# Kernel optimization log

Hardware: AMD Instinct MI355X
Metric: run time of the kernel (lower is better)

The kernel has to match this reference:

```python
import jax, jax.numpy as jnp
import numpy as np

EMB = 512
QKV = 512
H = 8      # num_heads
PH = 8     # num_pheads
HD = QKV // H
PHD = QKV // PH


def _make_params(key):
    names = ['Wi', 'Wip', 'Wic', 'Wq', 'Wpq', 'Wk', 'Wpk', 'Wv', 'Wpv', 'Wo', 'Wop']
    ks = jax.random.split(key, len(names))
    p = {}
    for n, k in zip(names, ks):
        din = EMB if n in ('Wi', 'Wip', 'Wic') else QKV
        dout = EMB if n in ('Wo', 'Wop') else QKV
        p[n] = jax.random.normal(k, (din, dout), jnp.float32) * 0.02
        p['b' + n[1:]] = jnp.zeros((dout,), jnp.float32)
    return p


def setup_inputs() -> dict:
    key = jax.random.key(0)
    kq, kp, kc, kw = jax.random.split(key, 4)
    B, S, P = 16, 4096, 64
    inp = {
        'query': jax.random.normal(kq, (B, S, EMB), jnp.float32),
        'pquery': jax.random.normal(kp, (B, P, EMB), jnp.float32),
        'context': jax.random.normal(kc, (B, S, EMB), jnp.float32),
    }
    inp.update(_make_params(kw))
    return inp


def reference(query, pquery, context,
              Wi, bi, Wip, bip, Wic, bic,
              Wq, bq, Wpq, bpq, Wk, bk, Wpk, bpk,
              Wv, bv, Wpv, bpv, Wo, bo, Wop, bop):
    # Dropout layers act as identity (eval mode / deterministic reference).
    B, S, _ = query.shape
    P = pquery.shape[1]

    q_in = query @ Wi + bi        # (B,S,QKV)
    pq_in = pquery @ Wip + bip    # (B,P,QKV)
    c_in = context @ Wic + bic    # (B,S,QKV)

    # --- pack stage: pquery attends over context -> p_context ---
    pq = ((pq_in @ Wpq + bpq) * (PHD ** -0.5)).reshape(B, P, PH, PHD)
    pk = (c_in @ Wpk + bpk).reshape(B, S, PH, PHD)
    pv = (c_in @ Wpv + bpv).reshape(B, S, PH, PHD)
    # dropout before softmax in original; identity here
    pattn = jax.nn.softmax(jnp.einsum('bphd,bshd->bhps', pq, pk), axis=-1)
    pc = jnp.einsum('bhps,bshd->bphd', pattn, pv).reshape(B, P, QKV)

    # --- unpack stage: query attends over p_context ---
    q = ((q_in @ Wq + bq) * (HD ** -0.5)).reshape(B, S, H, HD)
    k = (pc @ Wk + bk).reshape(B, P, H, HD)
    v = (pc @ Wv + bv).reshape(B, P, H, HD)
    aw = jax.nn.softmax(jnp.einsum('bshd,bphd->bhsp', q, k), axis=-1)  # (B,H,S,P)
    attn = jnp.einsum('bhsp,bphd->bshd', aw, v).reshape(B, S, QKV)
    attn = attn @ Wo + bo           # (B,S,EMB)
    pc_out = pc @ Wop + bop         # (B,P,EMB)

    # torch returns attn_weights as (S, B*H, P) when batch_first
    aw_t = jnp.transpose(aw.reshape(B * H, S, P), (1, 0, 2))
    return attn, pc_out, aw_t
```

## Files before the change

### kernel.cpp

```cpp
#include <hip/hip_runtime.h>


typedef __bf16 bf16x8 __attribute__((ext_vector_type(8)));
typedef float f32x4 __attribute__((ext_vector_type(4)));
typedef unsigned short u16x8 __attribute__((ext_vector_type(8)));
typedef unsigned short u16x4 __attribute__((ext_vector_type(4)));

#define MFMA16(a, b, c) __builtin_amdgcn_mfma_f32_16x16x32_bf16((a), (b), (c), 0, 0, 0)

__device__ __forceinline__ unsigned short f2bf_bits(float f) {
  unsigned int u = __float_as_uint(f);
  u += 0x7fffu + ((u >> 16) & 1u);
  return (unsigned short)(u >> 16);
}

__device__ __forceinline__ void gload16(const void* g, void* l) {
  __builtin_amdgcn_global_load_lds(
      (const __attribute__((address_space(1))) void*)g,
      (__attribute__((address_space(3))) void*)l, 16, 0, 0);
}

struct Ptr8 { const float* p[8]; };

__global__ __launch_bounds__(256) void prep_kernel(
    Ptr8 srcs, unsigned short* __restrict__ WT,
    const float* bi, const float* bip, const float* bic,
    const float* Wq, const float* Wpq, const float* Wpk, const float* Wpv,
    const float* bq, const float* bpq, const float* bpk, const float* bpv,
    float* __restrict__ bias_out) {
  const int t = threadIdx.x;
  if (blockIdx.z < 8) {
    const float* __restrict__ W = srcs.p[blockIdx.z];
    unsigned short* __restrict__ O = WT + (size_t)blockIdx.z * 262144;
    __shared__ float tile[32][33];
    const int tr = blockIdx.x * 32, tc = blockIdx.y * 32;
    {
      const int r = t >> 3, c4 = (t & 7) * 4;
      const float4 v = *reinterpret_cast<const float4*>(&W[(size_t)(tr + r) * 512 + tc + c4]);
      tile[r][c4 + 0] = v.x; tile[r][c4 + 1] = v.y; tile[r][c4 + 2] = v.z; tile[r][c4 + 3] = v.w;
    }
    __syncthreads();
    {
      const int n = t >> 3, k4 = (t & 7) * 4;
      u16x4 o;
#pragma unroll
      for (int j = 0; j < 4; j++) o[j] = f2bf_bits(tile[k4 + j][n]);
      *reinterpret_cast<u16x4*>(&O[(size_t)(tc + n) * 512 + tr + k4]) = o;
    }
  } else {
    const int idx = blockIdx.y * 16 + blockIdx.x;
    if (idx >= 8) return;
    const int y = idx >> 1;
    const float* bin  = (y == 0) ? bi : (y == 1) ? bip : bic;
    const float* W    = (y == 0) ? Wq : (y == 1) ? Wpq : (y == 2) ? Wpk : Wpv;
    const float* bout = (y == 0) ? bq : (y == 1) ? bpq : (y == 2) ? bpk : bpv;
    const float scale = (y < 2) ? 0.125f : 1.0f;
    const int n = (idx & 1) * 256 + t;
    float s = 0.f;
    for (int k = 0; k < 512; k++) s += bin[k] * W[(size_t)k * 512 + n];
    bias_out[y * 512 + n] = (s + bout[n]) * scale;
  }
}

__global__ __launch_bounds__(256) void gemm_wcomb(
    const float* __restrict__ Wi, const float* __restrict__ Wip,
    const float* __restrict__ Wic, const unsigned short* __restrict__ WTbase,
    unsigned short* __restrict__ outbase) {
  const int z = blockIdx.z;
  const float* __restrict__ A = (z == 0) ? Wi : (z == 1) ? Wip : Wic;
  const unsigned short* __restrict__ BT = WTbase + (size_t)z * 262144;
  unsigned short* __restrict__ out = outbase + (size_t)z * 262144;
  const float scale = (z < 2) ? 0.125f : 1.0f;

  __shared__ __align__(16) unsigned short As[128 * 72];
  __shared__ __align__(16) unsigned short Bs[128 * 72];
  const int t = threadIdx.x;
  const int w = t >> 6, l = t & 63, li = l & 15, lg = l >> 4;
  const int wm = w >> 1, wn = w & 1;
  const int m0 = blockIdx.x * 128, n0 = blockIdx.y * 128;

  f32x4 acc[4][4] = {};

  for (int kt = 0; kt < 512; kt += 64) {
#pragma unroll
    for (int i = 0; i < 8; i++) {
      const int row = i * 16 + (t >> 4), k = (t & 15) * 4;
      const float4 v = *reinterpret_cast<const float4*>(&A[(size_t)(m0 + row) * 512 + kt + k]);
      u16x4 o;
      o[0] = f2bf_bits(v.x); o[1] = f2bf_bits(v.y);
      o[2] = f2bf_bits(v.z); o[3] = f2bf_bits(v.w);
      *reinterpret_cast<u16x4*>(&As[row * 72 + k]) = o;
    }
#pragma unroll
    for (int i = 0; i < 4; i++) {
      const int row = i * 32 + (t >> 3), k = (t & 7) * 8;
      const u16x8 v = *reinterpret_cast<const u16x8*>(&BT[(size_t)(n0 + row) * 512 + kt + k]);
      *reinterpret_cast<u16x8*>(&Bs[row * 72 + k]) = v;
    }
    __syncthreads();
#pragma unroll
    for (int kk = 0; kk < 2; kk++) {
      bf16x8 a[4], b[4];
#pragma unroll
      for (int mf = 0; mf < 4; mf++)
        a[mf] = *reinterpret_cast<const bf16x8*>(&As[(wm * 64 + mf * 16 + li) * 72 + kk * 32 + lg * 8]);
#pragma unroll
      for (int nf = 0; nf < 4; nf++)
        b[nf] = *reinterpret_cast<const bf16x8*>(&Bs[(wn * 64 + nf * 16 + li) * 72 + kk * 32 + lg * 8]);
#pragma unroll
      for (int mf = 0; mf < 4; mf++)
#pragma unroll
        for (int nf = 0; nf < 4; nf++)
          acc[mf][nf] = MFMA16(a[mf], b[nf], acc[mf][nf]);
    }
    __syncthreads();
  }
  const int lg4 = lg * 4;
#pragma unroll
  for (int nf = 0; nf < 4; nf++) {
    const int col = n0 + wn * 64 + nf * 16 + li;
#pragma unroll
    for (int mf = 0; mf < 4; mf++) {
      const int row = m0 + wm * 64 + mf * 16 + lg4;
#pragma unroll
      for (int r = 0; r < 4; r++)
        out[(size_t)col * 512 + row + r] = f2bf_bits(acc[mf][nf][r] * scale);
    }
  }
}

__global__ __launch_bounds__(256) void gemm_f32lds(
    const float* __restrict__ A, const unsigned short* __restrict__ BT,
    const float* __restrict__ bias0, unsigned short* __restrict__ out0,
    int Ntiles, int ldc) {
  __shared__ __align__(16) float Asf[128 * 64];
  __shared__ __align__(16) unsigned short Bs[128 * 64];
  const int t = threadIdx.x;
  const int w = t >> 6, l = t & 63, li = l & 15, lg = l >> 4;
  const int wm = w >> 1, wn = w & 1;
  const int K = 512;

  const int q8 = gridDim.x >> 3;
  const int wg = (blockIdx.x & 7) * q8 + (blockIdx.x >> 3);
  const int m0 = (wg / Ntiles) * 128, n0 = (wg % Ntiles) * 128;

  f32x4 acc[4][4] = {};

  const int arow = t >> 4, aslot = t & 15;
  const int brow = t >> 3, bslot = t & 7;

  for (int kt = 0; kt < K; kt += 64) {
#pragma unroll
    for (int i = 0; i < 8; i++) {
      const int row = i * 16 + arow;
      const int gs = (aslot ^ (row & 15)) * 4;
      gload16(&A[(size_t)(m0 + row) * K + kt + gs], &Asf[i * 1024 + t * 4]);
    }
#pragma unroll
    for (int i = 0; i < 4; i++) {
      const int row = i * 32 + brow;
      const int gs = (bslot ^ (row & 7)) * 8;
      gload16(&BT[(size_t)(n0 + row) * K + kt + gs], &Bs[(i * 256 + t) * 8]);
    }
    __syncthreads();
#pragma unroll
    for (int kk = 0; kk < 2; kk++) {
      bf16x8 a[4], b[4];
#pragma unroll
      for (int mf = 0; mf < 4; mf++) {
        const int r = wm * 64 + mf * 16 + li;
        const int s0 = kk * 8 + lg * 2;
        const f32x4 lo = *reinterpret_cast<const f32x4*>(&Asf[r * 64 + ((s0 ^ (r & 15)) * 4)]);
        const f32x4 hi = *reinterpret_cast<const f32x4*>(&Asf[r * 64 + (((s0 + 1) ^ (r & 15)) * 4)]);
        bf16x8 v;
#pragma unroll
        for (int j = 0; j < 4; j++) { v[j] = (__bf16)lo[j]; v[j + 4] = (__bf16)hi[j]; }
        a[mf] = v;
      }
#pragma unroll
      for (int nf = 0; nf < 4; nf++) {
        const int r = wn * 64 + nf * 16 + li;
        b[nf] = *reinterpret_cast<const bf16x8*>(&Bs[r * 64 + (((kk * 4 + lg) ^ (r & 7)) * 8)]);
      }
#pragma unroll
      for (int mf = 0; mf < 4; mf++)
#pragma unroll
        for (int nf = 0; nf < 4; nf++)
          acc[mf][nf] = MFMA16(a[mf], b[nf], acc[mf][nf]);
    }
    __syncthreads();
  }

  const int lg4 = lg * 4;
#pragma unroll
  for (int nf = 0; nf < 4; nf++) {
    const int col = n0 + wn * 64 + nf * 16 + li;
    const float bv = bias0[col];
#pragma unroll
    for (int mf = 0; mf < 4; mf++) {
      const int row = m0 + wm * 64 + mf * 16 + lg4;
#pragma unroll
      for (int r = 0; r < 4; r++)
        out0[(size_t)(row + r) * ldc + col] = f2bf_bits(acc[mf][nf][r] + bv);
    }
  }
}

template <int MODE>
__global__ __launch_bounds__(256) void gemm_bf16(
    const unsigned short* __restrict__ A, const unsigned short* __restrict__ BT,
    const float* __restrict__ bias0, const float* __restrict__ bias1,
    const float* __restrict__ bias2, void* out0, void* out1, void* out2,
    int Ntiles, int ldc) {
  __shared__ __align__(16) unsigned short As[128 * 64];
  __shared__ __align__(16) unsigned short Bs[128 * 64];
  const int t = threadIdx.x;
  const int w = t >> 6, l = t & 63, li = l & 15, lg = l >> 4;
  const int wm = w >> 1, wn = w & 1;
  const int K = 512;

  const int q8 = gridDim.x >> 3;
  const int wg = (blockIdx.x & 7) * q8 + (blockIdx.x >> 3);
  const int m0 = (wg / Ntiles) * 128, n0 = (wg % Ntiles) * 128;

  f32x4 acc[4][4] = {};
  const int sr = t >> 3, sslot = t & 7;

  for (int kt = 0; kt < K; kt += 64) {
#pragma unroll
    for (int i = 0; i < 4; i++) {
      const int row = i * 32 + sr;
      const int gs = (sslot ^ (row & 7)) * 8;
      gload16(&A[(size_t)(m0 + row) * K + kt + gs], &As[(i * 256 + t) * 8]);
      gload16(&BT[(size_t)(n0 + row) * K + kt + gs], &Bs[(i * 256 + t) * 8]);
    }
    __syncthreads();
#pragma unroll
    for (int kk = 0; kk < 2; kk++) {
      bf16x8 a[4], b[4];
#pragma unroll
      for (int mf = 0; mf < 4; mf++) {
        const int r = wm * 64 + mf * 16 + li;
        a[mf] = *reinterpret_cast<const bf16x8*>(&As[r * 64 + (((kk * 4 + lg) ^ (r & 7)) * 8)]);
      }
#pragma unroll
      for (int nf = 0; nf < 4; nf++) {
        const int r = wn * 64 + nf * 16 + li;
        b[nf] = *reinterpret_cast<const bf16x8*>(&Bs[r * 64 + (((kk * 4 + lg) ^ (r & 7)) * 8)]);
      }
#pragma unroll
      for (int mf = 0; mf < 4; mf++)
#pragma unroll
        for (int nf = 0; nf < 4; nf++)
          acc[mf][nf] = MFMA16(a[mf], b[nf], acc[mf][nf]);
    }
    __syncthreads();
  }

  const int lg4 = lg * 4;
#pragma unroll
  for (int nf = 0; nf < 4; nf++) {
    const int col = n0 + wn * 64 + nf * 16 + li;
    if constexpr (MODE == 1) {
      float* o = (float*)out0;
      const float bv = bias0[col];
#pragma unroll
      for (int mf = 0; mf < 4; mf++) {
        const int row = m0 + wm * 64 + mf * 16 + lg4;
#pragma unroll
        for (int r = 0; r < 4; r++)
          o[(size_t)(row + r) * ldc + col] = acc[mf][nf][r] + bv;
      }
    } else {
      if (col < 512) {
        unsigned short* o = (unsigned short*)out0;
        const float bv = bias0[col];
#pragma unroll
        for (int mf = 0; mf < 4; mf++) {
          const int row = m0 + wm * 64 + mf * 16 + lg4;
#pragma unroll
          for (int r = 0; r < 4; r++)
            o[(size_t)(row + r) * 512 + col] = f2bf_bits(acc[mf][nf][r] + bv);
        }
      } else if (col < 1024) {
        unsigned short* o = (unsigned short*)out1;
        const float bv = bias1[col - 512];
#pragma unroll
        for (int mf = 0; mf < 4; mf++) {
          const int row = m0 + wm * 64 + mf * 16 + lg4;
#pragma unroll
          for (int r = 0; r < 4; r++)
            o[(size_t)(row + r) * 512 + col - 512] = f2bf_bits(acc[mf][nf][r] + bv);
        }
      } else {
        float* o = (float*)out2;
        const float bv = bias2[col - 1024];
#pragma unroll
        for (int mf = 0; mf < 4; mf++) {
          const int row = m0 + wm * 64 + mf * 16 + lg4;
#pragma unroll
          for (int r = 0; r < 4; r++)
            o[(size_t)(row + r) * 512 + col - 1024] = acc[mf][nf][r] + bv;
        }
      }
    }
  }
}

__global__ __launch_bounds__(256) void gemm_f32a(
    const float* __restrict__ A, const unsigned short* __restrict__ BT,
    const float* __restrict__ bias0, unsigned short* __restrict__ out,
    int K, int ldc) {
  __shared__ __align__(16) unsigned short As[128 * 72];
  __shared__ __align__(16) unsigned short Bs[128 * 72];
  const int t = threadIdx.x;
  const int w = t >> 6, l = t & 63, li = l & 15, lg = l >> 4;
  const int wm = w >> 1, wn = w & 1;
  const int m0 = blockIdx.x * 128, n0 = blockIdx.y * 128;

  f32x4 acc[4][4] = {};

  for (int kt = 0; kt < K; kt += 64) {
#pragma unroll
    for (int i = 0; i < 8; i++) {
      const int row = i * 16 + (t >> 4), k = (t & 15) * 4;
      const float4 v = *reinterpret_cast<const float4*>(&A[(size_t)(m0 + row) * K + kt + k]);
      u16x4 o;
      o[0] = f2bf_bits(v.x); o[1] = f2bf_bits(v.y);
      o[2] = f2bf_bits(v.z); o[3] = f2bf_bits(v.w);
      *reinterpret_cast<u16x4*>(&As[row * 72 + k]) = o;
    }
#pragma unroll
    for (int i = 0; i < 4; i++) {
      const int row = i * 32 + (t >> 3), k = (t & 7) * 8;
      const u16x8 v = *reinterpret_cast<const u16x8*>(&BT[(size_t)(n0 + row) * K + kt + k]);
      *reinterpret_cast<u16x8*>(&Bs[row * 72 + k]) = v;
    }
    __syncthreads();
#pragma unroll
    for (int kk = 0; kk < 2; kk++) {
      bf16x8 a[4], b[4];
#pragma unroll
      for (int mf = 0; mf < 4; mf++)
        a[mf] = *reinterpret_cast<const bf16x8*>(&As[(wm * 64 + mf * 16 + li) * 72 + kk * 32 + lg * 8]);
#pragma unroll
      for (int nf = 0; nf < 4; nf++)
        b[nf] = *reinterpret_cast<const bf16x8*>(&Bs[(wn * 64 + nf * 16 + li) * 72 + kk * 32 + lg * 8]);
#pragma unroll
      for (int mf = 0; mf < 4; mf++)
#pragma unroll
        for (int nf = 0; nf < 4; nf++)
          acc[mf][nf] = MFMA16(a[mf], b[nf], acc[mf][nf]);
    }
    __syncthreads();
  }
  const int lg4 = lg * 4;
#pragma unroll
  for (int nf = 0; nf < 4; nf++) {
    const int col = n0 + wn * 64 + nf * 16 + li;
    const float bv = bias0[col];
#pragma unroll
    for (int mf = 0; mf < 4; mf++) {
      const int row = m0 + wm * 64 + mf * 16 + lg4;
#pragma unroll
      for (int r = 0; r < 4; r++)
        out[(size_t)(row + r) * ldc + col] = f2bf_bits(acc[mf][nf][r] + bv);
    }
  }
}

__global__ __launch_bounds__(256) void pack_attn(
    const unsigned short* __restrict__ pq_buf,
    const unsigned short* __restrict__ pkv_buf, float* __restrict__ partial) {
  __shared__ __align__(16) unsigned short pkL[64 * 72];
  __shared__ __align__(16) unsigned short pvT[64 * 72];
  __shared__ __align__(16) unsigned short prL[4 * 16 * 72];
  const int t = threadIdx.x, w = t >> 6, l = t & 63, li = l & 15, lg = l >> 4;
  const int bh = blockIdx.x, b = bh >> 3, h = bh & 7;
  const int sb = blockIdx.y * 512;

  bf16x8 aq[2];
  {
    const size_t base = ((size_t)(b * 64 + w * 16 + li)) * 512 + h * 64;
    aq[0] = *reinterpret_cast<const bf16x8*>(&pq_buf[base + lg * 8]);
    aq[1] = *reinterpret_cast<const bf16x8*>(&pq_buf[base + 32 + lg * 8]);
  }

  f32x4 acc[4] = {};
  float lsum[4] = {};

  for (int st = 0; st < 8; st++) {
    const int s0 = sb + st * 64;
#pragma unroll
    for (int i = 0; i < 2; i++) {
      const int row = i * 32 + (t >> 3), c = (t & 7) * 8;
      const u16x8 v = *reinterpret_cast<const u16x8*>(
          &pkv_buf[((size_t)(b * 4096 + s0 + row)) * 1024 + h * 64 + c]);
      *reinterpret_cast<u16x8*>(&pkL[row * 72 + c]) = v;
    }
    {
      const int rp = t >> 3, c = (t & 7) * 8;
      const size_t base = ((size_t)(b * 4096 + s0 + 2 * rp)) * 1024 + 512 + h * 64 + c;
      const u16x8 u0 = *reinterpret_cast<const u16x8*>(&pkv_buf[base]);
      const u16x8 u1 = *reinterpret_cast<const u16x8*>(&pkv_buf[base + 1024]);
#pragma unroll
      for (int j = 0; j < 8; j++) {
        const int val = ((int)u0[j] & 0xffff) | ((int)u1[j] << 16);
        *reinterpret_cast<int*>(&pvT[(c + j) * 72 + 2 * rp]) = val;
      }
    }
    __syncthreads();
    f32x4 sc[4] = {};
#pragma unroll
    for (int nf = 0; nf < 4; nf++) {
#pragma unroll
      for (int kk = 0; kk < 2; kk++) {
        const bf16x8 bk = *reinterpret_cast<const bf16x8*>(
            &pkL[(nf * 16 + li) * 72 + kk * 32 + lg * 8]);
        sc[nf] = MFMA16(aq[kk], bk, sc[nf]);
      }
    }
#pragma unroll
    for (int nf = 0; nf < 4; nf++) {
#pragma unroll
      for (int r = 0; r < 4; r++) {
        const float e = __expf(sc[nf][r]);
        lsum[r] += e;
        prL[(w * 16 + lg * 4 + r) * 72 + nf * 16 + li] = f2bf_bits(e);
      }
    }
#pragma unroll
    for (int kk = 0; kk < 2; kk++) {
      const bf16x8 ap = *reinterpret_cast<const bf16x8*>(
          &prL[(w * 16 + li) * 72 + kk * 32 + lg * 8]);
#pragma unroll
      for (int nf = 0; nf < 4; nf++) {
        const bf16x8 bv = *reinterpret_cast<const bf16x8*>(
            &pvT[(nf * 16 + li) * 72 + kk * 32 + lg * 8]);
        acc[nf] = MFMA16(ap, bv, acc[nf]);
      }
    }
    __syncthreads();
  }

#pragma unroll
  for (int m = 1; m < 16; m <<= 1)
#pragma unroll
    for (int r = 0; r < 4; r++) lsum[r] += __shfl_xor(lsum[r], m);

  const size_t pbase = ((size_t)(bh * 8 + blockIdx.y)) * 4160;
#pragma unroll
  for (int nf = 0; nf < 4; nf++)
#pragma unroll
    for (int r = 0; r < 4; r++)
      partial[pbase + (size_t)(w * 16 + lg * 4 + r) * 64 + nf * 16 + li] = acc[nf][r];
  if (li == 0)
#pragma unroll
    for (int r = 0; r < 4; r++) partial[pbase + 4096 + w * 16 + lg * 4 + r] = lsum[r];
}

__global__ __launch_bounds__(256) void pack_combine(const float* __restrict__ partial,
                                                    unsigned short* __restrict__ pc_buf) {
  const int bh = blockIdx.x, b = bh >> 3, h = bh & 7;
  const int t = threadIdx.x;
#pragma unroll
  for (int e = 0; e < 16; e++) {
    const int idx = e * 256 + t;
    const int p = idx >> 6, d = idx & 63;
    float s = 0.f, den = 0.f;
#pragma unroll
    for (int c = 0; c < 8; c++) {
      const float* pb = &partial[((size_t)(bh * 8 + c)) * 4160];
      s += pb[idx];
      den += pb[4096 + p];
    }
    pc_buf[((size_t)(b * 64 + p)) * 512 + h * 64 + d] = f2bf_bits(s / den);
  }
}

__global__ __launch_bounds__(256) void unpack_attn(
    const unsigned short* q_in, const unsigned short* __restrict__ k_buf,
    const unsigned short* __restrict__ v_buf, float* __restrict__ aw_out,
    unsigned short* attnh_out) {
  __shared__ __align__(16) unsigned short kL[64 * 72];
  __shared__ __align__(16) unsigned short vT[64 * 72];
  __shared__ __align__(16) unsigned short prL[4 * 64 * 72];
  const int t = threadIdx.x, w = t >> 6, l = t & 63, li = l & 15, lg = l >> 4;
  const int bh = blockIdx.y, b = bh >> 3, h = bh & 7;
  const int sbase = blockIdx.x * 256 + w * 64;

#pragma unroll
  for (int i = 0; i < 2; i++) {
    const int p = i * 32 + (t >> 3), c = (t & 7) * 8;
    const u16x8 v = *reinterpret_cast<const u16x8*>(
        &k_buf[((size_t)(b * 64 + p)) * 512 + h * 64 + c]);
    *reinterpret_cast<u16x8*>(&kL[p * 72 + c]) = v;
  }
  {
    const int rp = t >> 3, c = (t & 7) * 8;
    const size_t base = ((size_t)(b * 64 + 2 * rp)) * 512 + h * 64 + c;
    const u16x8 u0 = *reinterpret_cast<const u16x8*>(&v_buf[base]);
    const u16x8 u1 = *reinterpret_cast<const u16x8*>(&v_buf[base + 512]);
#pragma unroll
    for (int j = 0; j < 8; j++) {
      const int val = ((int)u0[j] & 0xffff) | ((int)u1[j] << 16);
      *reinterpret_cast<int*>(&vT[(c + j) * 72 + 2 * rp]) = val;
    }
  }
  bf16x8 aq[4][2];
#pragma unroll
  for (int mf = 0; mf < 4; mf++) {
    const size_t base = ((size_t)(b * 4096 + sbase + mf * 16 + li)) * 512 + h * 64;
    aq[mf][0] = *reinterpret_cast<const bf16x8*>(&q_in[base + lg * 8]);
    aq[mf][1] = *reinterpret_cast<const bf16x8*>(&q_in[base + 32 + lg * 8]);
  }
  __syncthreads();

  f32x4 sc[4][4] = {};
#pragma unroll
  for (int kk = 0; kk < 2; kk++)
#pragma unroll
    for (int nf = 0; nf < 4; nf++) {
      const bf16x8 bk = *reinterpret_cast<const bf16x8*>(
          &kL[(nf * 16 + li) * 72 + kk * 32 + lg * 8]);
#pragma unroll
      for (int mf = 0; mf < 4; mf++) sc[mf][nf] = MFMA16(aq[mf][kk], bk, sc[mf][nf]);
    }

#pragma unroll
  for (int mf = 0; mf < 4; mf++) {
#pragma unroll
    for (int r = 0; r < 4; r++) {
      float e[4];
      float rs = 0.f;
#pragma unroll
      for (int nf = 0; nf < 4; nf++) {
        e[nf] = __expf(sc[mf][nf][r]);
        rs += e[nf];
      }
#pragma unroll
      for (int m = 1; m < 16; m <<= 1) rs += __shfl_xor(rs, m);
      const float inv = 1.0f / rs;
      const int srow = sbase + mf * 16 + lg * 4 + r;
#pragma unroll
      for (int nf = 0; nf < 4; nf++) {
        const float pr = e[nf] * inv;
        aw_out[(size_t)srow * 8192 + bh * 64 + nf * 16 + li] = pr;
        prL[(w * 64 + mf * 16 + lg * 4 + r) * 72 + nf * 16 + li] = f2bf_bits(pr);
      }
    }
  }

  f32x4 acc[4][4] = {};
#pragma unroll
  for (int kk = 0; kk < 2; kk++)
#pragma unroll
    for (int mf = 0; mf < 4; mf++) {
      const bf16x8 ap = *reinterpret_cast<const bf16x8*>(
          &prL[(w * 64 + mf * 16 + li) * 72 + kk * 32 + lg * 8]);
#pragma unroll
      for (int nf = 0; nf < 4; nf++) {
        const bf16x8 bv = *reinterpret_cast<const bf16x8*>(
            &vT[(nf * 16 + li) * 72 + kk * 32 + lg * 8]);
        acc[mf][nf] = MFMA16(ap, bv, acc[mf][nf]);
      }
    }
#pragma unroll
  for (int mf = 0; mf < 4; mf++)
#pragma unroll
    for (int nf = 0; nf < 4; nf++)
#pragma unroll
      for (int r = 0; r < 4; r++)
        attnh_out[((size_t)(b * 4096 + sbase + mf * 16 + lg * 4 + r)) * 512 + h * 64 +
                  nf * 16 + li] = f2bf_bits(acc[mf][nf][r]);
}

extern "C" void kernel_launch(void* const* d_in, const int* in_sizes, int n_in,
                              void* d_out, int out_size, void* d_ws, size_t ws_size,
                              hipStream_t stream) {
  (void)in_sizes; (void)n_in; (void)out_size; (void)ws_size;

  const float* query   = (const float*)d_in[0];
  const float* pquery  = (const float*)d_in[1];
  const float* context = (const float*)d_in[2];
  const float* Wi  = (const float*)d_in[3];  const float* bi  = (const float*)d_in[4];
  const float* Wip = (const float*)d_in[5];  const float* bip = (const float*)d_in[6];
  const float* Wic = (const float*)d_in[7];  const float* bic = (const float*)d_in[8];
  const float* Wq  = (const float*)d_in[9];  const float* bq  = (const float*)d_in[10];
  const float* Wpq = (const float*)d_in[11]; const float* bpq = (const float*)d_in[12];
  const float* Wk  = (const float*)d_in[13]; const float* bk  = (const float*)d_in[14];
  const float* Wpk = (const float*)d_in[15]; const float* bpk = (const float*)d_in[16];
  const float* Wv  = (const float*)d_in[17]; const float* bv  = (const float*)d_in[18];
  const float* Wpv = (const float*)d_in[19]; const float* bpv = (const float*)d_in[20];
  const float* Wo  = (const float*)d_in[21]; const float* bo  = (const float*)d_in[22];
  const float* Wop = (const float*)d_in[23]; const float* bop = (const float*)d_in[24];

  char* ws = (char*)d_ws;
  unsigned short* WT     = (unsigned short*)(ws);
  unsigned short* WqeT   = (unsigned short*)(ws + 4u * 1024 * 1024);
  unsigned short* WpqeT  = WqeT + 512 * 512;
  unsigned short* WpkveT = WpqeT + 512 * 512;
  float* bqe   = (float*)(WpkveT + (size_t)1024 * 512);
  float* bpqe  = bqe + 512;
  float* bpkve = bpqe + 512;
  unsigned short* q_buf   = (unsigned short*)(ws + 8u * 1024 * 1024);
  unsigned short* pkv_buf = q_buf + (size_t)65536 * 512;
  unsigned short* pq_buf  = pkv_buf + (size_t)65536 * 1024;
  unsigned short* pc_buf  = pq_buf + (size_t)1024 * 512;
  unsigned short* k_buf   = pc_buf + (size_t)1024 * 512;
  unsigned short* v_buf   = k_buf + (size_t)1024 * 512;
  float* partial = (float*)(v_buf + (size_t)1024 * 512);

  float* out_attn = (float*)d_out;
  float* out_pc   = out_attn + (size_t)16 * 4096 * 512;
  float* out_aw   = out_pc + (size_t)16 * 64 * 512;

  const dim3 blk(256);

  Ptr8 tsrc; tsrc.p[0]=Wq; tsrc.p[1]=Wpq; tsrc.p[2]=Wpk; tsrc.p[3]=Wpv;
  tsrc.p[4]=Wk; tsrc.p[5]=Wv; tsrc.p[6]=Wop; tsrc.p[7]=Wo;
  prep_kernel<<<dim3(16, 16, 9), blk, 0, stream>>>(
      tsrc, WT, bi, bip, bic, Wq, Wpq, Wpk, Wpv, bq, bpq, bpk, bpv, bqe);
  gemm_wcomb<<<dim3(4, 4, 4), blk, 0, stream>>>(Wi, Wip, Wic, WT, WqeT);

  gemm_f32lds<<<dim3(2048), blk, 0, stream>>>(query, WqeT, bqe, q_buf, 4, 512);
  gemm_f32lds<<<dim3(4096), blk, 0, stream>>>(context, WpkveT, bpkve, pkv_buf, 8, 1024);
  gemm_f32a<<<dim3(8, 4), blk, 0, stream>>>(pquery, WpqeT, bpqe, pq_buf, 512, 512);

  pack_attn<<<dim3(128, 8), blk, 0, stream>>>(pq_buf, pkv_buf, partial);
  pack_combine<<<128, blk, 0, stream>>>(partial, pc_buf);

  gemm_bf16<2><<<dim3(96), blk, 0, stream>>>(
      pc_buf, WT + (size_t)4 * 262144, bk, bv, bop, k_buf, v_buf, out_pc, 12, 512);

  unpack_attn<<<dim3(16, 128), blk, 0, stream>>>(q_buf, k_buf, v_buf, out_aw, q_buf);

  gemm_bf16<1><<<dim3(2048), blk, 0, stream>>>(
      q_buf, WT + (size_t)7 * 262144, bo, nullptr, nullptr, out_attn, nullptr, nullptr,
      4, 512);
}
```

Baseline: 525.7 us.

## Double-buffer LDS in large GEMMs and convert fp32 A to bf16 via registers

The three big GEMMs (query and context projections, output projection) now use double-buffered LDS tiles, so the next k-tile's global loads are issued before the MFMA work on the current tile. For fp32 inputs, A is loaded into registers, converted to bf16 and written into a swizzled bf16 LDS tile after compute, replacing fp32 LDS staging and the per-fragment conversion in the inner loop. This halves A's LDS footprint per buffer and moves conversion off the MFMA path, at the cost of more registers and two LDS buffers, which may lower occupancy. The small k/v/pc GEMM is split into its own non-templated kernel without block swizzling.

New measurement: 540.9 us. +2.9%, slower.

```diff
diff --git a/kernel.cpp b/kernel.cpp
--- a/kernel.cpp
+++ b/kernel.cpp
@@ -129,58 +129,78 @@
   }
 }
 
-__global__ __launch_bounds__(256) void gemm_f32lds(
+__global__ __launch_bounds__(256) void gemm2ph_f32a(
     const float* __restrict__ A, const unsigned short* __restrict__ BT,
     const float* __restrict__ bias0, unsigned short* __restrict__ out0,
     int Ntiles, int ldc) {
-  __shared__ __align__(16) float Asf[128 * 64];
-  __shared__ __align__(16) unsigned short Bs[128 * 64];
+  __shared__ __align__(16) unsigned short As[2][128 * 64];
+  __shared__ __align__(16) unsigned short Bs[2][128 * 64];
   const int t = threadIdx.x;
   const int w = t >> 6, l = t & 63, li = l & 15, lg = l >> 4;
   const int wm = w >> 1, wn = w & 1;
   const int K = 512;
-
   const int q8 = gridDim.x >> 3;
   const int wg = (blockIdx.x & 7) * q8 + (blockIdx.x >> 3);
   const int m0 = (wg / Ntiles) * 128, n0 = (wg % Ntiles) * 128;
 
   f32x4 acc[4][4] = {};
-
-  const int arow = t >> 4, aslot = t & 15;
+  const int arow = t >> 4, ac = t & 15;
   const int brow = t >> 3, bslot = t & 7;
-
-  for (int kt = 0; kt < K; kt += 64) {
-#pragma unroll
-    for (int i = 0; i < 8; i++) {
-      const int row = i * 16 + arow;
-      const int gs = (aslot ^ (row & 15)) * 4;
-      gload16(&A[(size_t)(m0 + row) * K + kt + gs], &Asf[i * 1024 + t * 4]);
-    }
-#pragma unroll
-    for (int i = 0; i < 4; i++) {
-      const int row = i * 32 + brow;
-      const int gs = (bslot ^ (row & 7)) * 8;
-      gload16(&BT[(size_t)(n0 + row) * K + kt + gs], &Bs[(i * 256 + t) * 8]);
-    }
-    __syncthreads();
+  float4 areg[8];
+
+#define ISSUE_A(kt)                                                            \
+  {                                                                            \
+    _Pragma("unroll") for (int i = 0; i < 8; i++)                              \
+        areg[i] = *reinterpret_cast<const float4*>(                            \
+            &A[(size_t)(m0 + i * 16 + arow) * K + (kt) + ac * 4]);             \
+  }
+#define STAGE_B(kt, buf)                                                       \
+  {                                                                            \
+    _Pragma("unroll") for (int i = 0; i < 4; i++) {                            \
+      const int row = i * 32 + brow;                                           \
+      const int gs = (bslot ^ (row & 7)) * 8;                                  \
+      gload16(&BT[(size_t)(n0 + row) * K + (kt) + gs], &Bs[buf][(i * 256 + t) * 8]); \
+    }                                                                          \
+  }
+#define WRITE_A(buf)                                                           \
+  {                                                                            \
+    _Pragma("unroll") for (int i = 0; i < 8; i++) {                            \
+      const int row = i * 16 + arow;                                           \
+      u16x4 o;                                                                 \
+      o[0] = f2bf_bits(areg[i].x); o[1] = f2bf_bits(areg[i].y);                \
+      o[2] = f2bf_bits(areg[i].z); o[3] = f2bf_bits(areg[i].w);                \
+      *reinterpret_cast<u16x4*>(                                               \
+          &As[buf][row * 64 + (((ac >> 1) ^ (row & 7)) * 8) + (ac & 1) * 4]) = o; \
+    }                                                                          \
+  }
+
+  ISSUE_A(0);
+  STAGE_B(0, 0);
+  WRITE_A(0);
+  __syncthreads();
+
+#pragma unroll 2
+  for (int tt = 0; tt < 8; tt++) {
+    const int cur = tt & 1, nxt = cur ^ 1;
+    const int ktn = (tt + 1) * 64;
+    if (tt < 7) {
+      STAGE_B(ktn, nxt);
+      ISSUE_A(ktn);
+    }
 #pragma unroll
     for (int kk = 0; kk < 2; kk++) {
       bf16x8 a[4], b[4];
 #pragma unroll
       for (int mf = 0; mf < 4; mf++) {
         const int r = wm * 64 + mf * 16 + li;
-        const int s0 = kk * 8 + lg * 2;
-        const f32x4 lo = *reinterpret_cast<const f32x4*>(&Asf[r * 64 + ((s0 ^ (r & 15)) * 4)]);
-        const f32x4 hi = *reinterpret_cast<const f32x4*>(&Asf[r * 64 + (((s0 + 1) ^ (r & 15)) * 4)]);
-        bf16x8 v;
-#pragma unroll
-        for (int j = 0; j < 4; j++) { v[j] = (__bf16)lo[j]; v[j + 4] = (__bf16)hi[j]; }
-        a[mf] = v;
+        a[mf] = *reinterpret_cast<const bf16x8*>(
+            &As[cur][r * 64 + (((kk * 4 + lg) ^ (r & 7)) * 8)]);
       }
 #pragma unroll
       for (int nf = 0; nf < 4; nf++) {
         const int r = wn * 64 + nf * 16 + li;
-        b[nf] = *reinterpret_cast<const bf16x8*>(&Bs[r * 64 + (((kk * 4 + lg) ^ (r & 7)) * 8)]);
+        b[nf] = *reinterpret_cast<const bf16x8*>(
+            &Bs[cur][r * 64 + (((kk * 4 + lg) ^ (r & 7)) * 8)]);
       }
 #pragma unroll
       for (int mf = 0; mf < 4; mf++)
@@ -188,8 +208,12 @@
         for (int nf = 0; nf < 4; nf++)
           acc[mf][nf] = MFMA16(a[mf], b[nf], acc[mf][nf]);
     }
-    __syncthreads();
-  }
+    if (tt < 7) WRITE_A(nxt);
+    __syncthreads();
+  }
+#undef ISSUE_A
+#undef STAGE_B
+#undef WRITE_A
 
   const int lg4 = lg * 4;
 #pragma unroll
@@ -206,22 +230,92 @@
   }
 }
 
-template <int MODE>
-__global__ __launch_bounds__(256) void gemm_bf16(
+__global__ __launch_bounds__(256) void gemm2ph_bf16f(
+    const unsigned short* __restrict__ A, const unsigned short* __restrict__ BT,
+    const float* __restrict__ bias0, float* __restrict__ out0,
+    int Ntiles, int ldc) {
+  __shared__ __align__(16) unsigned short As[2][128 * 64];
+  __shared__ __align__(16) unsigned short Bs[2][128 * 64];
+  const int t = threadIdx.x;
+  const int w = t >> 6, l = t & 63, li = l & 15, lg = l >> 4;
+  const int wm = w >> 1, wn = w & 1;
+  const int K = 512;
+  const int q8 = gridDim.x >> 3;
+  const int wg = (blockIdx.x & 7) * q8 + (blockIdx.x >> 3);
+  const int m0 = (wg / Ntiles) * 128, n0 = (wg % Ntiles) * 128;
+
+  f32x4 acc[4][4] = {};
+  const int sr = t >> 3, sslot = t & 7;
+
+#define STAGE_AB(kt, buf)                                                      \
+  {                                                                            \
+    _Pragma("unroll") for (int i = 0; i < 4; i++) {                            \
+      const int row = i * 32 + sr;                                             \
+      const int gs = (sslot ^ (row & 7)) * 8;                                  \
+      gload16(&A[(size_t)(m0 + row) * K + (kt) + gs], &As[buf][(i * 256 + t) * 8]); \
+      gload16(&BT[(size_t)(n0 + row) * K + (kt) + gs], &Bs[buf][(i * 256 + t) * 8]); \
+    }                                                                          \
+  }
+
+  STAGE_AB(0, 0);
+  __syncthreads();
+
+#pragma unroll 2
+  for (int tt = 0; tt < 8; tt++) {
+    const int cur = tt & 1, nxt = cur ^ 1;
+    if (tt < 7) STAGE_AB((tt + 1) * 64, nxt);
+#pragma unroll
+    for (int kk = 0; kk < 2; kk++) {
+      bf16x8 a[4], b[4];
+#pragma unroll
+      for (int mf = 0; mf < 4; mf++) {
+        const int r = wm * 64 + mf * 16 + li;
+        a[mf] = *reinterpret_cast<const bf16x8*>(
+            &As[cur][r * 64 + (((kk * 4 + lg) ^ (r & 7)) * 8)]);
+      }
+#pragma unroll
+      for (int nf = 0; nf < 4; nf++) {
+        const int r = wn * 64 + nf * 16 + li;
+        b[nf] = *reinterpret_cast<const bf16x8*>(
+            &Bs[cur][r * 64 + (((kk * 4 + lg) ^ (r & 7)) * 8)]);
+      }
+#pragma unroll
+      for (int mf = 0; mf < 4; mf++)
+#pragma unroll
+        for (int nf = 0; nf < 4; nf++)
+          acc[mf][nf] = MFMA16(a[mf], b[nf], acc[mf][nf]);
+    }
+    __syncthreads();
+  }
+#undef STAGE_AB
+
+  const int lg4 = lg * 4;
+#pragma unroll
+  for (int nf = 0; nf < 4; nf++) {
+    const int col = n0 + wn * 64 + nf * 16 + li;
+    const float bv = bias0[col];
+#pragma unroll
+    for (int mf = 0; mf < 4; mf++) {
+      const int row = m0 + wm * 64 + mf * 16 + lg4;
+#pragma unroll
+      for (int r = 0; r < 4; r++)
+        out0[(size_t)(row + r) * ldc + col] = acc[mf][nf][r] + bv;
+    }
+  }
+}
+
+__global__ __launch_bounds__(256) void gemm_kvpc(
     const unsigned short* __restrict__ A, const unsigned short* __restrict__ BT,
     const float* __restrict__ bias0, const float* __restrict__ bias1,
-    const float* __restrict__ bias2, void* out0, void* out1, void* out2,
-    int Ntiles, int ldc) {
+    const float* __restrict__ bias2, unsigned short* out0, unsigned short* out1,
+    float* out2, int Ntiles) {
   __shared__ __align__(16) unsigned short As[128 * 64];
   __shared__ __align__(16) unsigned short Bs[128 * 64];
   const int t = threadIdx.x;
   const int w = t >> 6, l = t & 63, li = l & 15, lg = l >> 4;
   const int wm = w >> 1, wn = w & 1;
   const int K = 512;
-
-  const int q8 = gridDim.x >> 3;
-  const int wg = (blockIdx.x & 7) * q8 + (blockIdx.x >> 3);
-  const int m0 = (wg / Ntiles) * 128, n0 = (wg % Ntiles) * 128;
+  const int m0 = (blockIdx.x / Ntiles) * 128, n0 = (blockIdx.x % Ntiles) * 128;
 
   f32x4 acc[4][4] = {};
   const int sr = t >> 3, sslot = t & 7;
@@ -261,47 +355,32 @@
 #pragma unroll
   for (int nf = 0; nf < 4; nf++) {
     const int col = n0 + wn * 64 + nf * 16 + li;
-    if constexpr (MODE == 1) {
-      float* o = (float*)out0;
+    if (col < 512) {
       const float bv = bias0[col];
 #pragma unroll
       for (int mf = 0; mf < 4; mf++) {
         const int row = m0 + wm * 64 + mf * 16 + lg4;
 #pragma unroll
         for (int r = 0; r < 4; r++)
-          o[(size_t)(row + r) * ldc + col] = acc[mf][nf][r] + bv;
+          out0[(size_t)(row + r) * 512 + col] = f2bf_bits(acc[mf][nf][r] + bv);
+      }
+    } else if (col < 1024) {
+      const float bv = bias1[col - 512];
+#pragma unroll
+      for (int mf = 0; mf < 4; mf++) {
+        const int row = m0 + wm * 64 + mf * 16 + lg4;
+#pragma unroll
+        for (int r = 0; r < 4; r++)
+          out1[(size_t)(row + r) * 512 + col - 512] = f2bf_bits(acc[mf][nf][r] + bv);
       }
     } else {
-      if (col < 512) {
-        unsigned short* o = (unsigned short*)out0;
-        const float bv = bias0[col];
-#pragma unroll
-        for (int mf = 0; mf < 4; mf++) {
-          const int row = m0 + wm * 64 + mf * 16 + lg4;
-#pragma unroll
-          for (int r = 0; r < 4; r++)
-            o[(size_t)(row + r) * 512 + col] = f2bf_bits(acc[mf][nf][r] + bv);
-        }
-      } else if (col < 1024) {
-        unsigned short* o = (unsigned short*)out1;
-        const float bv = bias1[col - 512];
-#pragma unroll
-        for (int mf = 0; mf < 4; mf++) {
-          const int row = m0 + wm * 64 + mf * 16 + lg4;
-#pragma unroll
-          for (int r = 0; r < 4; r++)
-            o[(size_t)(row + r) * 512 + col - 512] = f2bf_bits(acc[mf][nf][r] + bv);
-        }
-      } else {
-        float* o = (float*)out2;
-        const float bv = bias2[col - 1024];
-#pragma unroll
-        for (int mf = 0; mf < 4; mf++) {
-          const int row = m0 + wm * 64 + mf * 16 + lg4;
-#pragma unroll
-          for (int r = 0; r < 4; r++)
-            o[(size_t)(row + r) * 512 + col - 1024] = acc[mf][nf][r] + bv;
-        }
+      const float bv = bias2[col - 1024];
+#pragma unroll
+      for (int mf = 0; mf < 4; mf++) {
+        const int row = m0 + wm * 64 + mf * 16 + lg4;
+#pragma unroll
+        for (int r = 0; r < 4; r++)
+          out2[(size_t)(row + r) * 512 + col - 1024] = acc[mf][nf][r] + bv;
       }
     }
   }
@@ -623,19 +702,18 @@
       tsrc, WT, bi, bip, bic, Wq, Wpq, Wpk, Wpv, bq, bpq, bpk, bpv, bqe);
   gemm_wcomb<<<dim3(4, 4, 4), blk, 0, stream>>>(Wi, Wip, Wic, WT, WqeT);
 
-  gemm_f32lds<<<dim3(2048), blk, 0, stream>>>(query, WqeT, bqe, q_buf, 4, 512);
-  gemm_f32lds<<<dim3(4096), blk, 0, stream>>>(context, WpkveT, bpkve, pkv_buf, 8, 1024);
+  gemm2ph_f32a<<<dim3(2048), blk, 0, stream>>>(query, WqeT, bqe, q_buf, 4, 512);
+  gemm2ph_f32a<<<dim3(4096), blk, 0, stream>>>(context, WpkveT, bpkve, pkv_buf, 8, 1024);
   gemm_f32a<<<dim3(8, 4), blk, 0, stream>>>(pquery, WpqeT, bpqe, pq_buf, 512, 512);
 
   pack_attn<<<dim3(128, 8), blk, 0, stream>>>(pq_buf, pkv_buf, partial);
   pack_combine<<<128, blk, 0, stream>>>(partial, pc_buf);
 
-  gemm_bf16<2><<<dim3(96), blk, 0, stream>>>(
-      pc_buf, WT + (size_t)4 * 262144, bk, bv, bop, k_buf, v_buf, out_pc, 12, 512);
+  gemm_kvpc<<<dim3(96), blk, 0, stream>>>(
+      pc_buf, WT + (size_t)4 * 262144, bk, bv, bop, k_buf, v_buf, out_pc, 12);
 
   unpack_attn<<<dim3(16, 128), blk, 0, stream>>>(q_buf, k_buf, v_buf, out_aw, q_buf);
 
-  gemm_bf16<1><<<dim3(2048), blk, 0, stream>>>(
-      q_buf, WT + (size_t)7 * 262144, bo, nullptr, nullptr, out_attn, nullptr, nullptr,
-      4, 512);
-}
+  gemm2ph_bf16f<<<dim3(2048), blk, 0, stream>>>(
+      q_buf, WT + (size_t)7 * 262144, bo, out_attn, 4, 512);
+}
```

## Use double-buffered BK=32 GEMM pipeline and merge three input projections into one launch

Applied to the files above, without the earlier changes.

Replaces the single-buffered BK=64 GEMM kernels with a two-stage pipeline over K=32 slices. The next B tile is staged via global_load_lds and the next A tile is prefetched into registers while MFMAs run on the current buffer. The input projections for query, context and pquery now run in one grouped launch, and the output projection uses the same pipelined body. The smaller LDS footprint and launch_bounds(256,4) aim for higher occupancy and better latency hiding, at the cost of more barriers per K and conversion of f32 A through registers.

New measurement: 504.8 us. -4.0%, faster.

```diff
diff --git a/kernel.cpp b/kernel.cpp
--- a/kernel.cpp
+++ b/kernel.cpp
@@ -129,99 +129,161 @@
   }
 }
 
-__global__ __launch_bounds__(256) void gemm_f32lds(
-    const float* __restrict__ A, const unsigned short* __restrict__ BT,
-    const float* __restrict__ bias0, unsigned short* __restrict__ out0,
-    int Ntiles, int ldc) {
-  __shared__ __align__(16) float Asf[128 * 64];
-  __shared__ __align__(16) unsigned short Bs[128 * 64];
+template <typename AT, int OUTF32>
+__device__ __forceinline__ void gemm2ph_body(
+    const AT* __restrict__ A, const unsigned short* __restrict__ BT,
+    const float* __restrict__ bias, void* out, int Ntiles, int ldc, int wg) {
+  __shared__ __align__(16) unsigned short As[2][128 * 40];
+  __shared__ __align__(16) unsigned short Bs[2][128 * 32];
   const int t = threadIdx.x;
   const int w = t >> 6, l = t & 63, li = l & 15, lg = l >> 4;
   const int wm = w >> 1, wn = w & 1;
   const int K = 512;
-
-  const int q8 = gridDim.x >> 3;
-  const int wg = (blockIdx.x & 7) * q8 + (blockIdx.x >> 3);
   const int m0 = (wg / Ntiles) * 128, n0 = (wg % Ntiles) * 128;
 
   f32x4 acc[4][4] = {};
-
-  const int arow = t >> 4, aslot = t & 15;
-  const int brow = t >> 3, bslot = t & 7;
-
-  for (int kt = 0; kt < K; kt += 64) {
-#pragma unroll
-    for (int i = 0; i < 8; i++) {
-      const int row = i * 16 + arow;
-      const int gs = (aslot ^ (row & 15)) * 4;
-      gload16(&A[(size_t)(m0 + row) * K + kt + gs], &Asf[i * 1024 + t * 4]);
-    }
-#pragma unroll
-    for (int i = 0; i < 4; i++) {
-      const int row = i * 32 + brow;
-      const int gs = (bslot ^ (row & 7)) * 8;
-      gload16(&BT[(size_t)(n0 + row) * K + kt + gs], &Bs[(i * 256 + t) * 8]);
-    }
-    __syncthreads();
-#pragma unroll
-    for (int kk = 0; kk < 2; kk++) {
-      bf16x8 a[4], b[4];
-#pragma unroll
-      for (int mf = 0; mf < 4; mf++) {
-        const int r = wm * 64 + mf * 16 + li;
-        const int s0 = kk * 8 + lg * 2;
-        const f32x4 lo = *reinterpret_cast<const f32x4*>(&Asf[r * 64 + ((s0 ^ (r & 15)) * 4)]);
-        const f32x4 hi = *reinterpret_cast<const f32x4*>(&Asf[r * 64 + (((s0 + 1) ^ (r & 15)) * 4)]);
-        bf16x8 v;
-#pragma unroll
-        for (int j = 0; j < 4; j++) { v[j] = (__bf16)lo[j]; v[j + 4] = (__bf16)hi[j]; }
-        a[mf] = v;
-      }
-#pragma unroll
-      for (int nf = 0; nf < 4; nf++) {
-        const int r = wn * 64 + nf * 16 + li;
-        b[nf] = *reinterpret_cast<const bf16x8*>(&Bs[r * 64 + (((kk * 4 + lg) ^ (r & 7)) * 8)]);
-      }
-#pragma unroll
-      for (int mf = 0; mf < 4; mf++)
-#pragma unroll
-        for (int nf = 0; nf < 4; nf++)
-          acc[mf][nf] = MFMA16(a[mf], b[nf], acc[mf][nf]);
-    }
-    __syncthreads();
-  }
+  float4 aregf[4];
+  u16x8 aregh[2];
+  const int brow_ = t >> 2, bslot_ = t & 3;
+
+#define ISSUE_A(kt)                                                            \
+  if constexpr (sizeof(AT) == 4) {                                             \
+    _Pragma("unroll") for (int i = 0; i < 4; i++)                              \
+        aregf[i] = *reinterpret_cast<const float4*>(                           \
+            &A[(size_t)(m0 + i * 32 + (t >> 3)) * K + (kt) + (t & 7) * 4]);    \
+  } else {                                                                     \
+    _Pragma("unroll") for (int i = 0; i < 2; i++)                              \
+        aregh[i] = *reinterpret_cast<const u16x8*>(                            \
+            &A[(size_t)(m0 + i * 64 + (t >> 2)) * K + (kt) + (t & 3) * 8]);    \
+  }
+
+#define WRITE_A(buf)                                                           \
+  if constexpr (sizeof(AT) == 4) {                                             \
+    _Pragma("unroll") for (int i = 0; i < 4; i++) {                            \
+      const int row = i * 32 + (t >> 3);                                       \
+      u16x4 o;                                                                 \
+      o[0] = f2bf_bits(aregf[i].x); o[1] = f2bf_bits(aregf[i].y);              \
+      o[2] = f2bf_bits(aregf[i].z); o[3] = f2bf_bits(aregf[i].w);              \
+      *reinterpret_cast<u16x4*>(&As[buf][row * 40 + (t & 7) * 4]) = o;         \
+    }                                                                          \
+  } else {                                                                     \
+    _Pragma("unroll") for (int i = 0; i < 2; i++) {                            \
+      const int row = i * 64 + (t >> 2);                                       \
+      *reinterpret_cast<u16x8*>(&As[buf][row * 40 + (t & 3) * 8]) = aregh[i];  \
+    }                                                                          \
+  }
+
+#define STAGE_B(kt, buf)                                                       \
+  {                                                                            \
+    _Pragma("unroll") for (int i = 0; i < 2; i++) {                            \
+      const int row = i * 64 + brow_;                                          \
+      const int gs = (bslot_ ^ ((row >> 1) & 3)) * 8;                          \
+      gload16(&BT[(size_t)(n0 + row) * K + (kt) + gs],                         \
+              &Bs[buf][i * 2048 + t * 8]);                                     \
+    }                                                                          \
+  }
+
+  ISSUE_A(0);
+  STAGE_B(0, 0);
+  WRITE_A(0);
+  __syncthreads();
+
+#pragma unroll 2
+  for (int tt = 0; tt < 16; tt++) {
+    const int cur = tt & 1, nxt = cur ^ 1;
+    if (tt < 15) {
+      STAGE_B((tt + 1) * 32, nxt);
+      ISSUE_A((tt + 1) * 32);
+    }
+    bf16x8 a[4], b[4];
+#pragma unroll
+    for (int mf = 0; mf < 4; mf++) {
+      const int r = wm * 64 + mf * 16 + li;
+      a[mf] = *reinterpret_cast<const bf16x8*>(&As[cur][r * 40 + lg * 8]);
+    }
+#pragma unroll
+    for (int nf = 0; nf < 4; nf++) {
+      const int r = wn * 64 + nf * 16 + li;
+      b[nf] = *reinterpret_cast<const bf16x8*>(
+          &Bs[cur][r * 32 + ((lg ^ ((r >> 1) & 3)) * 8)]);
+    }
+#pragma unroll
+    for (int mf = 0; mf < 4; mf++)
+#pragma unroll
+      for (int nf = 0; nf < 4; nf++)
+        acc[mf][nf] = MFMA16(a[mf], b[nf], acc[mf][nf]);
+    if (tt < 15) WRITE_A(nxt);
+    __syncthreads();
+  }
+#undef ISSUE_A
+#undef WRITE_A
+#undef STAGE_B
 
   const int lg4 = lg * 4;
 #pragma unroll
   for (int nf = 0; nf < 4; nf++) {
     const int col = n0 + wn * 64 + nf * 16 + li;
-    const float bv = bias0[col];
+    const float bv = bias[col];
 #pragma unroll
     for (int mf = 0; mf < 4; mf++) {
       const int row = m0 + wm * 64 + mf * 16 + lg4;
-#pragma unroll
-      for (int r = 0; r < 4; r++)
-        out0[(size_t)(row + r) * ldc + col] = f2bf_bits(acc[mf][nf][r] + bv);
-    }
-  }
-}
-
-template <int MODE>
-__global__ __launch_bounds__(256) void gemm_bf16(
+      if constexpr (OUTF32) {
+        float* o = (float*)out;
+#pragma unroll
+        for (int r = 0; r < 4; r++)
+          o[(size_t)(row + r) * ldc + col] = acc[mf][nf][r] + bv;
+      } else {
+        unsigned short* o = (unsigned short*)out;
+#pragma unroll
+        for (int r = 0; r < 4; r++)
+          o[(size_t)(row + r) * ldc + col] = f2bf_bits(acc[mf][nf][r] + bv);
+      }
+    }
+  }
+}
+
+__global__ __launch_bounds__(256, 4) void gemm2ph_qpkv(
+    const float* query, const float* context, const float* pquery,
+    const unsigned short* WqeT, const unsigned short* WpkveT,
+    const unsigned short* WpqeT, const float* bqe, const float* bpkve,
+    const float* bpqe, unsigned short* q_buf, unsigned short* pkv_buf,
+    unsigned short* pq_buf) {
+  const int q8 = gridDim.x >> 3;
+  int wg = ((int)blockIdx.x & 7) * q8 + ((int)blockIdx.x >> 3);
+  const float* A; const unsigned short* BT; const float* bias;
+  unsigned short* out; int Ntiles, ldc;
+  if (wg < 2048) {
+    A = query; BT = WqeT; bias = bqe; out = q_buf; Ntiles = 4; ldc = 512;
+  } else if (wg < 6144) {
+    wg -= 2048; A = context; BT = WpkveT; bias = bpkve; out = pkv_buf;
+    Ntiles = 8; ldc = 1024;
+  } else {
+    wg -= 6144; A = pquery; BT = WpqeT; bias = bpqe; out = pq_buf;
+    Ntiles = 4; ldc = 512;
+  }
+  gemm2ph_body<float, 0>(A, BT, bias, out, Ntiles, ldc, wg);
+}
+
+__global__ __launch_bounds__(256, 4) void gemm2ph_final(
+    const unsigned short* A, const unsigned short* BT, const float* bias,
+    float* out) {
+  const int q8 = gridDim.x >> 3;
+  const int wg = ((int)blockIdx.x & 7) * q8 + ((int)blockIdx.x >> 3);
+  gemm2ph_body<unsigned short, 1>(A, BT, bias, out, 4, 512, wg);
+}
+
+__global__ __launch_bounds__(256) void gemm_kvpc(
     const unsigned short* __restrict__ A, const unsigned short* __restrict__ BT,
     const float* __restrict__ bias0, const float* __restrict__ bias1,
-    const float* __restrict__ bias2, void* out0, void* out1, void* out2,
-    int Ntiles, int ldc) {
+    const float* __restrict__ bias2, unsigned short* out0, unsigned short* out1,
+    float* out2, int Ntiles) {
   __shared__ __align__(16) unsigned short As[128 * 64];
   __shared__ __align__(16) unsigned short Bs[128 * 64];
   const int t = threadIdx.x;
   const int w = t >> 6, l = t & 63, li = l & 15, lg = l >> 4;
   const int wm = w >> 1, wn = w & 1;
   const int K = 512;
-
-  const int q8 = gridDim.x >> 3;
-  const int wg = (blockIdx.x & 7) * q8 + (blockIdx.x >> 3);
-  const int m0 = (wg / Ntiles) * 128, n0 = (wg % Ntiles) * 128;
+  const int m0 = (blockIdx.x / Ntiles) * 128, n0 = (blockIdx.x % Ntiles) * 128;
 
   f32x4 acc[4][4] = {};
   const int sr = t >> 3, sslot = t & 7;
@@ -261,110 +323,33 @@
 #pragma unroll
   for (int nf = 0; nf < 4; nf++) {
     const int col = n0 + wn * 64 + nf * 16 + li;
-    if constexpr (MODE == 1) {
-      float* o = (float*)out0;
+    if (col < 512) {
       const float bv = bias0[col];
 #pragma unroll
       for (int mf = 0; mf < 4; mf++) {
         const int row = m0 + wm * 64 + mf * 16 + lg4;
 #pragma unroll
         for (int r = 0; r < 4; r++)
-          o[(size_t)(row + r) * ldc + col] = acc[mf][nf][r] + bv;
+          out0[(size_t)(row + r) * 512 + col] = f2bf_bits(acc[mf][nf][r] + bv);
+      }
+    } else if (col < 1024) {
+      const float bv = bias1[col - 512];
+#pragma unroll
+      for (int mf = 0; mf < 4; mf++) {
+        const int row = m0 + wm * 64 + mf * 16 + lg4;
+#pragma unroll
+        for (int r = 0; r < 4; r++)
+          out1[(size_t)(row + r) * 512 + col - 512] = f2bf_bits(acc[mf][nf][r] + bv);
       }
     } else {
-      if (col < 512) {
-        unsigned short* o = (unsigned short*)out0;
-        const float bv = bias0[col];
-#pragma unroll
-        for (int mf = 0; mf < 4; mf++) {
-          const int row = m0 + wm * 64 + mf * 16 + lg4;
-#pragma unroll
-          for (int r = 0; r < 4; r++)
-            o[(size_t)(row + r) * 512 + col] = f2bf_bits(acc[mf][nf][r] + bv);
-        }
-      } else if (col < 1024) {
-        unsigned short* o = (unsigned short*)out1;
-        const float bv = bias1[col - 512];
-#pragma unroll
-        for (int mf = 0; mf < 4; mf++) {
-          const int row = m0 + wm * 64 + mf * 16 + lg4;
-#pragma unroll
-          for (int r = 0; r < 4; r++)
-            o[(size_t)(row + r) * 512 + col - 512] = f2bf_bits(acc[mf][nf][r] + bv);
-        }
-      } else {
-        float* o = (float*)out2;
-        const float bv = bias2[col - 1024];
-#pragma unroll
-        for (int mf = 0; mf < 4; mf++) {
-          const int row = m0 + wm * 64 + mf * 16 + lg4;
-#pragma unroll
-          for (int r = 0; r < 4; r++)
-            o[(size_t)(row + r) * 512 + col - 1024] = acc[mf][nf][r] + bv;
-        }
-      }
-    }
-  }
-}
-
-__global__ __launch_bounds__(256) void gemm_f32a(
-    const float* __restrict__ A, const unsigned short* __restrict__ BT,
-    const float* __restrict__ bias0, unsigned short* __restrict__ out,
-    int K, int ldc) {
-  __shared__ __align__(16) unsigned short As[128 * 72];
-  __shared__ __align__(16) unsigned short Bs[128 * 72];
-  const int t = threadIdx.x;
-  const int w = t >> 6, l = t & 63, li = l & 15, lg = l >> 4;
-  const int wm = w >> 1, wn = w & 1;
-  const int m0 = blockIdx.x * 128, n0 = blockIdx.y * 128;
-
-  f32x4 acc[4][4] = {};
-
-  for (int kt = 0; kt < K; kt += 64) {
-#pragma unroll
-    for (int i = 0; i < 8; i++) {
-      const int row = i * 16 + (t >> 4), k = (t & 15) * 4;
-      const float4 v = *reinterpret_cast<const float4*>(&A[(size_t)(m0 + row) * K + kt + k]);
-      u16x4 o;
-      o[0] = f2bf_bits(v.x); o[1] = f2bf_bits(v.y);
-      o[2] = f2bf_bits(v.z); o[3] = f2bf_bits(v.w);
-      *reinterpret_cast<u16x4*>(&As[row * 72 + k]) = o;
-    }
-#pragma unroll
-    for (int i = 0; i < 4; i++) {
-      const int row = i * 32 + (t >> 3), k = (t & 7) * 8;
-      const u16x8 v = *reinterpret_cast<const u16x8*>(&BT[(size_t)(n0 + row) * K + kt + k]);
-      *reinterpret_cast<u16x8*>(&Bs[row * 72 + k]) = v;
-    }
-    __syncthreads();
-#pragma unroll
-    for (int kk = 0; kk < 2; kk++) {
-      bf16x8 a[4], b[4];
-#pragma unroll
-      for (int mf = 0; mf < 4; mf++)
-        a[mf] = *reinterpret_cast<const bf16x8*>(&As[(wm * 64 + mf * 16 + li) * 72 + kk * 32 + lg * 8]);
-#pragma unroll
-      for (int nf = 0; nf < 4; nf++)
-        b[nf] = *reinterpret_cast<const bf16x8*>(&Bs[(wn * 64 + nf * 16 + li) * 72 + kk * 32 + lg * 8]);
-#pragma unroll
-      for (int mf = 0; mf < 4; mf++)
-#pragma unroll
-        for (int nf = 0; nf < 4; nf++)
-          acc[mf][nf] = MFMA16(a[mf], b[nf], acc[mf][nf]);
-    }
-    __syncthreads();
-  }
-  const int lg4 = lg * 4;
-#pragma unroll
-  for (int nf = 0; nf < 4; nf++) {
-    const int col = n0 + wn * 64 + nf * 16 + li;
-    const float bv = bias0[col];
-#pragma unroll
-    for (int mf = 0; mf < 4; mf++) {
-      const int row = m0 + wm * 64 + mf * 16 + lg4;
-#pragma unroll
-      for (int r = 0; r < 4; r++)
-        out[(size_t)(row + r) * ldc + col] = f2bf_bits(acc[mf][nf][r] + bv);
+      const float bv = bias2[col - 1024];
+#pragma unroll
+      for (int mf = 0; mf < 4; mf++) {
+        const int row = m0 + wm * 64 + mf * 16 + lg4;
+#pragma unroll
+        for (int r = 0; r < 4; r++)
+          out2[(size_t)(row + r) * 512 + col - 1024] = acc[mf][nf][r] + bv;
+      }
     }
   }
 }
@@ -623,19 +608,18 @@
       tsrc, WT, bi, bip, bic, Wq, Wpq, Wpk, Wpv, bq, bpq, bpk, bpv, bqe);
   gemm_wcomb<<<dim3(4, 4, 4), blk, 0, stream>>>(Wi, Wip, Wic, WT, WqeT);
 
-  gemm_f32lds<<<dim3(2048), blk, 0, stream>>>(query, WqeT, bqe, q_buf, 4, 512);
-  gemm_f32lds<<<dim3(4096), blk, 0, stream>>>(context, WpkveT, bpkve, pkv_buf, 8, 1024);
-  gemm_f32a<<<dim3(8, 4), blk, 0, stream>>>(pquery, WpqeT, bpqe, pq_buf, 512, 512);
+  gemm2ph_qpkv<<<dim3(6176), blk, 0, stream>>>(
+      query, context, pquery, WqeT, WpkveT, WpqeT, bqe, bpkve, bpqe,
+      q_buf, pkv_buf, pq_buf);
 
   pack_attn<<<dim3(128, 8), blk, 0, stream>>>(pq_buf, pkv_buf, partial);
   pack_combine<<<128, blk, 0, stream>>>(partial, pc_buf);
 
-  gemm_bf16<2><<<dim3(96), blk, 0, stream>>>(
-      pc_buf, WT + (size_t)4 * 262144, bk, bv, bop, k_buf, v_buf, out_pc, 12, 512);
+  gemm_kvpc<<<dim3(96), blk, 0, stream>>>(
+      pc_buf, WT + (size_t)4 * 262144, bk, bv, bop, k_buf, v_buf, out_pc, 12);
 
   unpack_attn<<<dim3(16, 128), blk, 0, stream>>>(q_buf, k_buf, v_buf, out_aw, q_buf);
 
-  gemm_bf16<1><<<dim3(2048), blk, 0, stream>>>(
-      q_buf, WT + (size_t)7 * 262144, bo, nullptr, nullptr, out_attn, nullptr, nullptr,
-      4, 512);
-}
+  gemm2ph_final<<<dim3(2048), blk, 0, stream>>>(
+      q_buf, WT + (size_t)7 * 262144, bo, out_attn);
+}
```
